# Performance work log

Hardware: AMD Instinct MI355X
Metric: run time of the kernel (lower is better)

Reference implementation:

```python
import jax, jax.numpy as jnp
import numpy as np

D_MODEL = 1024
NUM_HEADS = 16
D_LATENT = 256
HEAD_DIM = D_MODEL // NUM_HEADS
BATCH = 2048
SEQ = 32


def setup_inputs() -> dict:
    key = jax.random.key(0)
    ks = jax.random.split(key, 9)
    s = 1.0 / np.sqrt(D_MODEL)
    sl = 1.0 / np.sqrt(D_LATENT)
    return {
        "x": jax.random.normal(ks[0], (BATCH, SEQ, D_MODEL), dtype=jnp.float32),
        "memory": jax.random.normal(ks[1], (BATCH, SEQ, D_LATENT), dtype=jnp.float32),
        "W_q": jax.random.normal(ks[2], (D_MODEL, D_MODEL), dtype=jnp.float32) * s,
        "W_k": jax.random.normal(ks[3], (D_MODEL, D_MODEL), dtype=jnp.float32) * s,
        "W_v": jax.random.normal(ks[4], (D_MODEL, D_MODEL), dtype=jnp.float32) * s,
        "W_o": jax.random.normal(ks[5], (D_MODEL, D_MODEL), dtype=jnp.float32) * s,
        "W_down_kv": jax.random.normal(ks[6], (D_MODEL, D_LATENT), dtype=jnp.float32) * s,
        "W_up_k": jax.random.normal(ks[7], (D_LATENT, D_MODEL), dtype=jnp.float32) * sl,
        "W_up_v": jax.random.normal(ks[8], (D_LATENT, D_MODEL), dtype=jnp.float32) * sl,
    }


def reference(x, memory, W_q, W_k, W_v, W_o, W_down_kv, W_up_k, W_up_v):
    B, S, _ = x.shape
    q = x @ W_q                     # [B,S,D]
    k = x @ W_k
    v = x @ W_v
    latent_kv = (k + v) @ W_down_kv  # [B,S,L]
    latent_kv = jnp.nan_to_num((latent_kv + memory) * 0.5)
    k_rec = latent_kv @ W_up_k       # [B,S,D]
    v_rec = latent_kv @ W_up_v
    # split heads: [B,H,S,hd]
    qh = q.reshape(B, S, NUM_HEADS, HEAD_DIM).transpose(0, 2, 1, 3)
    kh = k_rec.reshape(B, S, NUM_HEADS, HEAD_DIM).transpose(0, 2, 1, 3)
    vh = v_rec.reshape(B, S, NUM_HEADS, HEAD_DIM).transpose(0, 2, 1, 3)
    # NOTE: faithful to source — scale is sqrt(d_model), not sqrt(head_dim)
    scores = jnp.einsum("bhqd,bhkd->bhqk", qh, kh) / jnp.sqrt(jnp.float32(D_MODEL))
    scores = jnp.nan_to_num(scores, nan=0.0, posinf=10.0, neginf=-10.0)
    attn = jax.nn.softmax(scores, axis=-1)
    ctx = jnp.einsum("bhqk,bhkd->bhqd", attn, vh)
    ctx = ctx.transpose(0, 2, 1, 3).reshape(B, S, D_MODEL)
    out = ctx @ W_o
    return out, latent_kv
```

## Files before the change

### kernel.cpp

```cpp
#include <hip/hip_runtime.h>
#include <hip/hip_bf16.h>

typedef unsigned short u16;
typedef __attribute__((ext_vector_type(8))) __bf16 bf16x8;
typedef __attribute__((ext_vector_type(8))) unsigned short u16x8;
typedef __attribute__((ext_vector_type(4))) float floatx4;
typedef __attribute__((ext_vector_type(16))) float floatx16;

#define AS1 __attribute__((address_space(1)))
#define AS3 __attribute__((address_space(3)))

__device__ __forceinline__ u16 f2bf(float f) {
  unsigned u = __float_as_uint(f);
  u += 0x7fffu + ((u >> 16) & 1u);
  return (u16)(u >> 16);
}

__device__ __forceinline__ void g2lds16(const u16* g, u16* l) {
  __builtin_amdgcn_global_load_lds((AS1 void*)g, (AS3 void*)l, 16, 0, 0);
}

__global__ __launch_bounds__(256) void k_cvt_bf16(const float* __restrict__ s,
                                                  u16* __restrict__ d, long n) {
  long i = ((long)blockIdx.x * blockDim.x + threadIdx.x) * 8;
  long stride = (long)gridDim.x * blockDim.x * 8;
  for (; i < n; i += stride) {
    float4 a = *(const float4*)(s + i);
    float4 b = *(const float4*)(s + i + 4);
    u16x8 o;
    o[0] = f2bf(a.x); o[1] = f2bf(a.y); o[2] = f2bf(a.z); o[3] = f2bf(a.w);
    o[4] = f2bf(b.x); o[5] = f2bf(b.y); o[6] = f2bf(b.z); o[7] = f2bf(b.w);
    *(u16x8*)(d + i) = o;
  }
}

__global__ __launch_bounds__(256) void k_addcvt(const float* __restrict__ s0,
                                                const float* __restrict__ s1,
                                                u16* __restrict__ d, long n) {
  long i = ((long)blockIdx.x * blockDim.x + threadIdx.x) * 8;
  long stride = (long)gridDim.x * blockDim.x * 8;
  for (; i < n; i += stride) {
    float4 a0 = *(const float4*)(s0 + i);
    float4 a1 = *(const float4*)(s0 + i + 4);
    float4 b0 = *(const float4*)(s1 + i);
    float4 b1 = *(const float4*)(s1 + i + 4);
    u16x8 o;
    o[0] = f2bf(a0.x + b0.x); o[1] = f2bf(a0.y + b0.y);
    o[2] = f2bf(a0.z + b0.z); o[3] = f2bf(a0.w + b0.w);
    o[4] = f2bf(a1.x + b1.x); o[5] = f2bf(a1.y + b1.y);
    o[6] = f2bf(a1.z + b1.z); o[7] = f2bf(a1.w + b1.w);
    *(u16x8*)(d + i) = o;
  }
}

__global__ __launch_bounds__(256) void k_tcvt(const float* __restrict__ s,
                                              u16* __restrict__ d, int R, int C) {
  __shared__ float t[32][33];
  const int lx = threadIdx.x, ly = threadIdx.y;
  const int bx = blockIdx.x * 32;
  const int by = blockIdx.y * 32;
  #pragma unroll
  for (int i = 0; i < 32; i += 8)
    t[ly + i][lx] = s[(size_t)(by + ly + i) * C + bx + lx];
  __syncthreads();
  #pragma unroll
  for (int i = 0; i < 32; i += 8)
    d[(size_t)(bx + ly + i) * R + by + lx] = f2bf(t[lx][ly + i]);
}


#define MFMA16(a, b, c) c = __builtin_amdgcn_mfma_f32_16x16x32_bf16(a, b, c, 0, 0, 0)

#define STAGE(BUF, OP, RH, T) do {                                              \
    const u16* Gp_ = (OP) ? Bg : Ag;                                            \
    const u16* g0_ = Gp_ + (size_t)((RH) * 128 + srow) * K + (T) * 64 + scols;  \
    u16* L_ = ldsb + ((BUF) * 2 + (OP)) * 16384 + (RH) * 8192 + tid * 8;        \
    g2lds16(g0_, L_);                                                           \
    g2lds16(g0_ + (size_t)64 * K, L_ + 4096);                                   \
  } while (0)

#define RD_A(AI, F, KS) \
  (*(const bf16x8*)(LA + ((wr * 128 + (AI) * 64 + (F) * 16 + fr) * 64 + ((((KS) * 32) + g8) ^ xr))))
#define RD_B(BJ, NF, KS) \
  (*(const bf16x8*)(LB + ((wc * 64 + (BJ) * 32 + (NF) * 16 + fr) * 64 + ((((KS) * 32) + g8) ^ xr))))

#define PHASE_READS(AI, BJ)                                                       \
  bf16x8 pa0_0 = RD_A(AI, 0, 0), pa1_0 = RD_A(AI, 1, 0);                          \
  bf16x8 pa2_0 = RD_A(AI, 2, 0), pa3_0 = RD_A(AI, 3, 0);                          \
  bf16x8 pa0_1 = RD_A(AI, 0, 1), pa1_1 = RD_A(AI, 1, 1);                          \
  bf16x8 pa2_1 = RD_A(AI, 2, 1), pa3_1 = RD_A(AI, 3, 1);                          \
  bf16x8 pb0_0 = RD_B(BJ, 0, 0), pb1_0 = RD_B(BJ, 1, 0);                          \
  bf16x8 pb0_1 = RD_B(BJ, 0, 1), pb1_1 = RD_B(BJ, 1, 1)

#define PHASE_MFMA(AI, BJ)                                                        \
  __builtin_amdgcn_s_setprio(1);                                                  \
  MFMA16(pa0_0, pb0_0, acc[(AI)*4 + 0][(BJ)*2 + 0]);                              \
  MFMA16(pa1_0, pb0_0, acc[(AI)*4 + 1][(BJ)*2 + 0]);                              \
  MFMA16(pa2_0, pb0_0, acc[(AI)*4 + 2][(BJ)*2 + 0]);                              \
  MFMA16(pa3_0, pb0_0, acc[(AI)*4 + 3][(BJ)*2 + 0]);                              \
  MFMA16(pa0_0, pb1_0, acc[(AI)*4 + 0][(BJ)*2 + 1]);                              \
  MFMA16(pa1_0, pb1_0, acc[(AI)*4 + 1][(BJ)*2 + 1]);                              \
  MFMA16(pa2_0, pb1_0, acc[(AI)*4 + 2][(BJ)*2 + 1]);                              \
  MFMA16(pa3_0, pb1_0, acc[(AI)*4 + 3][(BJ)*2 + 1]);                              \
  MFMA16(pa0_1, pb0_1, acc[(AI)*4 + 0][(BJ)*2 + 0]);                              \
  MFMA16(pa1_1, pb0_1, acc[(AI)*4 + 1][(BJ)*2 + 0]);                              \
  MFMA16(pa2_1, pb0_1, acc[(AI)*4 + 2][(BJ)*2 + 0]);                              \
  MFMA16(pa3_1, pb0_1, acc[(AI)*4 + 3][(BJ)*2 + 0]);                              \
  MFMA16(pa0_1, pb1_1, acc[(AI)*4 + 0][(BJ)*2 + 1]);                              \
  MFMA16(pa1_1, pb1_1, acc[(AI)*4 + 1][(BJ)*2 + 1]);                              \
  MFMA16(pa2_1, pb1_1, acc[(AI)*4 + 2][(BJ)*2 + 1]);                              \
  MFMA16(pa3_1, pb1_1, acc[(AI)*4 + 3][(BJ)*2 + 1]);                              \
  __builtin_amdgcn_s_setprio(0)

template <int MODE>
__global__ __launch_bounds__(512, 2) void gemm8p(
    const u16* __restrict__ A, const u16* __restrict__ Bt,
    int M, int N, int K, int ntn,
    u16* __restrict__ Cb, float* __restrict__ Cf,
    const float* __restrict__ memp, float* __restrict__ latf, u16* __restrict__ latb) {
  extern __shared__ u16 ldsb[];
  const int tid = threadIdx.x;
  const int lane = tid & 63;
  const int wid = tid >> 6;
  const int wr = wid >> 2, wc = wid & 3;

  int bid = blockIdx.x;
  {
    const int nwg = gridDim.x;
    const int q = nwg >> 3, r = nwg & 7;
    const int xcd = bid & 7, idx = bid >> 3;
    bid = (xcd < r ? xcd * (q + 1) : r * (q + 1) + (xcd - r) * q) + idx;
  }
  const int mt = bid / ntn, nt = bid % ntn;
  const int m0 = mt * 256, n0 = nt * 256;
  const int NT = K >> 6;

  const int srow = tid >> 3;
  const int scols = ((tid & 7) ^ (srow & 7)) * 8;
  const int fr = lane & 15;
  const int g8 = (lane >> 4) * 8;
  const int xr = (lane & 7) * 8;

  const u16* Ag = A + (size_t)m0 * K;
  const u16* Bg = Bt + (size_t)n0 * K;

  floatx4 acc[8][4];
  #pragma unroll
  for (int i = 0; i < 8; i++)
    #pragma unroll
    for (int j = 0; j < 4; j++) acc[i][j] = 0.0f;

  STAGE(0, 0, 0, 0);
  STAGE(0, 0, 1, 0);
  STAGE(0, 1, 0, 0);
  STAGE(0, 1, 1, 0);
  if (NT > 1) {
    STAGE(1, 0, 0, 1);
    asm volatile("s_waitcnt vmcnt(2)" ::: "memory");
  } else {
    asm volatile("s_waitcnt vmcnt(0)" ::: "memory");
  }
  __builtin_amdgcn_s_barrier();

  for (int t = 0; t < NT; ++t) {
    const int cur = t & 1;
    const u16* LA = ldsb + cur * 32768;
    const u16* LB = LA + 16384;
    const int nxt = cur ^ 1;
    {
      PHASE_READS(0, 0);
      if (t + 1 < NT) STAGE(nxt, 0, 1, t + 1);
      __builtin_amdgcn_s_barrier();
      asm volatile("s_waitcnt lgkmcnt(0)" ::: "memory");
      PHASE_MFMA(0, 0);
      __builtin_amdgcn_s_barrier();
    }
    {
      PHASE_READS(0, 1);
      if (t + 1 < NT) STAGE(nxt, 1, 0, t + 1);
      __builtin_amdgcn_s_barrier();
      asm volatile("s_waitcnt lgkmcnt(0)" ::: "memory");
      PHASE_MFMA(0, 1);
      __builtin_amdgcn_s_barrier();
    }
    {
      PHASE_READS(1, 0);
      if (t + 1 < NT) STAGE(nxt, 1, 1, t + 1);
      __builtin_amdgcn_s_barrier();
      asm volatile("s_waitcnt lgkmcnt(0)" ::: "memory");
      PHASE_MFMA(1, 0);
      __builtin_amdgcn_s_barrier();
    }
    {
      PHASE_READS(1, 1);
      asm volatile("s_waitcnt lgkmcnt(0)" ::: "memory");
      __builtin_amdgcn_s_barrier();
      if (t + 2 < NT) STAGE(cur, 0, 0, t + 2);
      PHASE_MFMA(1, 1);
      if (t + 2 < NT) asm volatile("s_waitcnt vmcnt(2)" ::: "memory");
      else            asm volatile("s_waitcnt vmcnt(0)" ::: "memory");
      __builtin_amdgcn_s_barrier();
    }
  }

  #pragma unroll
  for (int mi = 0; mi < 8; mi++) {
    const int mb = m0 + wr * 128 + mi * 16 + ((lane >> 4) * 4);
    #pragma unroll
    for (int ni = 0; ni < 4; ni++) {
      const int cb = n0 + wc * 64 + ni * 16 + (lane & 15);
      #pragma unroll
      for (int r = 0; r < 4; r++) {
        const int m = mb + r;
        const float v = acc[mi][ni][r];
        if (MODE == 0) {
          Cb[(size_t)m * N + cb] = f2bf(v);
        } else if (MODE == 1) {
          if (n0 < 1024) {
            Cb[(size_t)m * 1024 + cb] = f2bf(v);
          } else {
            int lc = cb - 1024;
            float lv = (v + memp[(size_t)m * 256 + lc]) * 0.5f;
            latf[(size_t)m * 256 + lc] = lv;
            latb[(size_t)m * 256 + lc] = f2bf(lv);
          }
        } else {
          Cf[(size_t)m * N + cb] = v;
        }
      }
    }
  }
}

__global__ __launch_bounds__(256) void k_attn(const u16* __restrict__ KV, u16* Q) {
  __shared__ u16 Qs[4][32][72];
  __shared__ u16 Ks[4][32][72];
  __shared__ u16 Vt[4][64][40];
  const int tid = threadIdx.x;
  const int hg = blockIdx.x;
  const int b = blockIdx.y;
  const long tok0 = (long)b * 32;

  {
    const int t = tid >> 3, ci = tid & 7;
    const int hd = ci >> 1, c0 = (ci & 1) * 32;
    const u16* qrow = Q + (tok0 + t) * 1024 + hg * 256 + ci * 32;
    #pragma unroll
    for (int u = 0; u < 4; u++)
      *(u16x8*)&Qs[hd][t][c0 + u * 8] = *(const u16x8*)(qrow + u * 8);
    const u16* krow = KV + (tok0 + t) * 2048 + hg * 256 + ci * 32;
    #pragma unroll
    for (int u = 0; u < 4; u++)
      *(u16x8*)&Ks[hd][t][c0 + u * 8] = *(const u16x8*)(krow + u * 8);
    const u16* vrow = KV + (tok0 + t) * 2048 + 1024 + hg * 256 + ci * 32;
    #pragma unroll
    for (int u = 0; u < 4; u++) {
      u16x8 v = *(const u16x8*)(vrow + u * 8);
      #pragma unroll
      for (int j = 0; j < 8; j++) Vt[hd][c0 + u * 8 + j][t] = v[j];
    }
  }
  __syncthreads();

  const int w = tid >> 6;
  const int lane = tid & 63;
  const int col = lane & 31, hi = lane >> 5;

  floatx16 S;
  #pragma unroll
  for (int r = 0; r < 16; r++) S[r] = 0.0f;
  #pragma unroll
  for (int kc = 0; kc < 4; kc++) {
    bf16x8 aq = *(const bf16x8*)&Qs[w][col][kc * 16 + hi * 8];
    bf16x8 bk = *(const bf16x8*)&Ks[w][col][kc * 16 + hi * 8];
    S = __builtin_amdgcn_mfma_f32_32x32x16_bf16(aq, bk, S, 0, 0, 0);
  }

  u16* Pw = &Qs[w][0][0];
  float pr[16];
  #pragma unroll
  for (int r = 0; r < 16; r++) {
    float sc = S[r] * 0.03125f;
    float mx = sc;
    #pragma unroll
    for (int off = 16; off >= 1; off >>= 1) mx = fmaxf(mx, __shfl_xor(mx, off, 64));
    float e = __expf(sc - mx);
    float sm = e;
    #pragma unroll
    for (int off = 16; off >= 1; off >>= 1) sm += __shfl_xor(sm, off, 64);
    pr[r] = e / sm;
  }
  #pragma unroll
  for (int r = 0; r < 16; r++) {
    int row = (r & 3) + 8 * (r >> 2) + 4 * hi;
    Pw[row * 40 + col] = f2bf(pr[r]);
  }
  __syncthreads();

  floatx16 c0v, c1v;
  #pragma unroll
  for (int r = 0; r < 16; r++) { c0v[r] = 0.0f; c1v[r] = 0.0f; }
  #pragma unroll
  for (int kc = 0; kc < 2; kc++) {
    bf16x8 ap = *(const bf16x8*)&Pw[col * 40 + kc * 16 + hi * 8];
    bf16x8 bv0 = *(const bf16x8*)&Vt[w][col][kc * 16 + hi * 8];
    bf16x8 bv1 = *(const bf16x8*)&Vt[w][32 + col][kc * 16 + hi * 8];
    c0v = __builtin_amdgcn_mfma_f32_32x32x16_bf16(ap, bv0, c0v, 0, 0, 0);
    c1v = __builtin_amdgcn_mfma_f32_32x32x16_bf16(ap, bv1, c1v, 0, 0, 0);
  }
  #pragma unroll
  for (int r = 0; r < 16; r++) {
    int row = (r & 3) + 8 * (r >> 2) + 4 * hi;
    u16* orow = Q + (tok0 + row) * 1024 + hg * 256 + w * 64;
    orow[col] = f2bf(c0v[r]);
    orow[col + 32] = f2bf(c1v[r]);
  }
}

extern "C" void kernel_launch(void* const* d_in, const int* in_sizes, int n_in,
                              void* d_out, int out_size, void* d_ws, size_t ws_size,
                              hipStream_t stream) {
  const float* x    = (const float*)d_in[0];
  const float* mem  = (const float*)d_in[1];
  const float* W_q  = (const float*)d_in[2];
  const float* W_k  = (const float*)d_in[3];
  const float* W_v  = (const float*)d_in[4];
  const float* W_o  = (const float*)d_in[5];
  const float* W_dn = (const float*)d_in[6];
  const float* W_uk = (const float*)d_in[7];
  const float* W_uv = (const float*)d_in[8];
  float* out  = (float*)d_out;
  float* latf = out + (size_t)67108864;

  char* wp = (char*)d_ws;
  u16* Qb  = (u16*)wp; wp += (size_t)65536 * 1024 * 2;
  u16* Lb  = (u16*)wp; wp += (size_t)65536 * 256 * 2;
  u16* WAt = (u16*)wp; wp += (size_t)1280 * 1024 * 2;
  u16* WBt = (u16*)wp; wp += (size_t)2048 * 256 * 2;
  u16* Wot = (u16*)wp; wp += (size_t)1024 * 1024 * 2;
  u16* Wdt = (u16*)wp; wp += (size_t)256 * 1024 * 2;
  u16* Wkv = (u16*)wp; wp += (size_t)1024 * 1024 * 2;

  u16* Xb  = (u16*)d_out;
  u16* KVb = (u16*)d_out;

  (void)hipFuncSetAttribute(reinterpret_cast<const void*>(&gemm8p<0>),
                            hipFuncAttributeMaxDynamicSharedMemorySize, 131072);
  (void)hipFuncSetAttribute(reinterpret_cast<const void*>(&gemm8p<1>),
                            hipFuncAttributeMaxDynamicSharedMemorySize, 131072);
  (void)hipFuncSetAttribute(reinterpret_cast<const void*>(&gemm8p<2>),
                            hipFuncAttributeMaxDynamicSharedMemorySize, 131072);

  dim3 b256(256);
  dim3 b512(512);
  dim3 tb(32, 8);
  k_cvt_bf16<<<4096, b256, 0, stream>>>(x, Xb, (long)67108864);
  k_addcvt<<<512, b256, 0, stream>>>(W_k, W_v, Wkv, (long)1048576);
  k_tcvt<<<dim3(32, 32), tb, 0, stream>>>(W_q, WAt, 1024, 1024);
  k_tcvt<<<dim3(8, 32),  tb, 0, stream>>>(W_dn, Wdt, 1024, 256);
  k_tcvt<<<dim3(32, 8),  tb, 0, stream>>>(W_uk, WBt, 256, 1024);
  k_tcvt<<<dim3(32, 8),  tb, 0, stream>>>(W_uv, WBt + (size_t)1024 * 256, 256, 1024);
  k_tcvt<<<dim3(32, 32), tb, 0, stream>>>(W_o, Wot, 1024, 1024);

  gemm8p<0><<<4, b512, 131072, stream>>>(
      Wdt, Wkv, 256, 1024, 1024, 4, WAt + (size_t)1024 * 1024,
      nullptr, nullptr, nullptr, nullptr);

  gemm8p<1><<<1280, b512, 131072, stream>>>(
      Xb, WAt, 65536, 1280, 1024, 5, Qb, nullptr, mem, latf, Lb);

  gemm8p<0><<<2048, b512, 131072, stream>>>(
      Lb, WBt, 65536, 2048, 256, 8, KVb, nullptr, nullptr, nullptr, nullptr);

  k_attn<<<dim3(4, 2048), b256, 0, stream>>>(KVb, Qb);

  gemm8p<2><<<1024, b512, 131072, stream>>>(
      Qb, Wot, 65536, 1024, 1024, 4, nullptr, out, nullptr, nullptr, nullptr);
}
```

Baseline: 887.4 us.

## Hold B fragments in registers across phases and issue all next-tile loads upfront

Restructures the GEMM main loop so each wave reads its full set of B fragments once per K-tile and keeps them in registers. Each of the four phases now only reads two new A row-fragments, which cuts redundant LDS reads of B. The global-to-LDS prefetch of all four quadrants of the next tile is issued at the start of the iteration instead of being spread across phases, and the deeper two-tile prefetch (t+2 into the current buffer) is dropped. In exchange this raises register pressure and lowers the prefetch depth, which may expose global load latency at the end of each tile.

```diff
diff --git a/kernel.cpp b/kernel.cpp
--- a/kernel.cpp
+++ b/kernel.cpp
@@ -79,37 +79,29 @@
     g2lds16(g0_ + (size_t)64 * K, L_ + 4096);                                   \
   } while (0)
 
-#define RD_A(AI, F, KS) \
-  (*(const bf16x8*)(LA + ((wr * 128 + (AI) * 64 + (F) * 16 + fr) * 64 + ((((KS) * 32) + g8) ^ xr))))
-#define RD_B(BJ, NF, KS) \
-  (*(const bf16x8*)(LB + ((wc * 64 + (BJ) * 32 + (NF) * 16 + fr) * 64 + ((((KS) * 32) + g8) ^ xr))))
-
-#define PHASE_READS(AI, BJ)                                                       \
-  bf16x8 pa0_0 = RD_A(AI, 0, 0), pa1_0 = RD_A(AI, 1, 0);                          \
-  bf16x8 pa2_0 = RD_A(AI, 2, 0), pa3_0 = RD_A(AI, 3, 0);                          \
-  bf16x8 pa0_1 = RD_A(AI, 0, 1), pa1_1 = RD_A(AI, 1, 1);                          \
-  bf16x8 pa2_1 = RD_A(AI, 2, 1), pa3_1 = RD_A(AI, 3, 1);                          \
-  bf16x8 pb0_0 = RD_B(BJ, 0, 0), pb1_0 = RD_B(BJ, 1, 0);                          \
-  bf16x8 pb0_1 = RD_B(BJ, 0, 1), pb1_1 = RD_B(BJ, 1, 1)
-
-#define PHASE_MFMA(AI, BJ)                                                        \
-  __builtin_amdgcn_s_setprio(1);                                                  \
-  MFMA16(pa0_0, pb0_0, acc[(AI)*4 + 0][(BJ)*2 + 0]);                              \
-  MFMA16(pa1_0, pb0_0, acc[(AI)*4 + 1][(BJ)*2 + 0]);                              \
-  MFMA16(pa2_0, pb0_0, acc[(AI)*4 + 2][(BJ)*2 + 0]);                              \
-  MFMA16(pa3_0, pb0_0, acc[(AI)*4 + 3][(BJ)*2 + 0]);                              \
-  MFMA16(pa0_0, pb1_0, acc[(AI)*4 + 0][(BJ)*2 + 1]);                              \
-  MFMA16(pa1_0, pb1_0, acc[(AI)*4 + 1][(BJ)*2 + 1]);                              \
-  MFMA16(pa2_0, pb1_0, acc[(AI)*4 + 2][(BJ)*2 + 1]);                              \
-  MFMA16(pa3_0, pb1_0, acc[(AI)*4 + 3][(BJ)*2 + 1]);                              \
-  MFMA16(pa0_1, pb0_1, acc[(AI)*4 + 0][(BJ)*2 + 0]);                              \
-  MFMA16(pa1_1, pb0_1, acc[(AI)*4 + 1][(BJ)*2 + 0]);                              \
-  MFMA16(pa2_1, pb0_1, acc[(AI)*4 + 2][(BJ)*2 + 0]);                              \
-  MFMA16(pa3_1, pb0_1, acc[(AI)*4 + 3][(BJ)*2 + 0]);                              \
-  MFMA16(pa0_1, pb1_1, acc[(AI)*4 + 0][(BJ)*2 + 1]);                              \
-  MFMA16(pa1_1, pb1_1, acc[(AI)*4 + 1][(BJ)*2 + 1]);                              \
-  MFMA16(pa2_1, pb1_1, acc[(AI)*4 + 2][(BJ)*2 + 1]);                              \
-  MFMA16(pa3_1, pb1_1, acc[(AI)*4 + 3][(BJ)*2 + 1]);                              \
+#define RD_A2(MI, KS) \
+  (*(const bf16x8*)(LA + ((wr * 128 + (MI) * 16 + fr) * 64 + ((((KS) * 32) + g8) ^ xr))))
+#define RD_B2(NI, KS) \
+  (*(const bf16x8*)(LB + ((wc * 64 + (NI) * 16 + fr) * 64 + ((((KS) * 32) + g8) ^ xr))))
+
+#define PH_MFMA(MI0)                                         \
+  __builtin_amdgcn_s_setprio(1);                             \
+  MFMA16(a0[0], Br[0][0], acc[MI0][0]);                      \
+  MFMA16(a1[0], Br[0][0], acc[(MI0) + 1][0]);                \
+  MFMA16(a0[0], Br[1][0], acc[MI0][1]);                      \
+  MFMA16(a1[0], Br[1][0], acc[(MI0) + 1][1]);                \
+  MFMA16(a0[0], Br[2][0], acc[MI0][2]);                      \
+  MFMA16(a1[0], Br[2][0], acc[(MI0) + 1][2]);                \
+  MFMA16(a0[0], Br[3][0], acc[MI0][3]);                      \
+  MFMA16(a1[0], Br[3][0], acc[(MI0) + 1][3]);                \
+  MFMA16(a0[1], Br[0][1], acc[MI0][0]);                      \
+  MFMA16(a1[1], Br[0][1], acc[(MI0) + 1][0]);                \
+  MFMA16(a0[1], Br[1][1], acc[MI0][1]);                      \
+  MFMA16(a1[1], Br[1][1], acc[(MI0) + 1][1]);                \
+  MFMA16(a0[1], Br[2][1], acc[MI0][2]);                      \
+  MFMA16(a1[1], Br[2][1], acc[(MI0) + 1][2]);                \
+  MFMA16(a0[1], Br[3][1], acc[MI0][3]);                      \
+  MFMA16(a1[1], Br[3][1], acc[(MI0) + 1][3]);                \
   __builtin_amdgcn_s_setprio(0)
 
 template <int MODE>
@@ -154,51 +146,56 @@
   STAGE(0, 0, 1, 0);
   STAGE(0, 1, 0, 0);
   STAGE(0, 1, 1, 0);
-  if (NT > 1) {
-    STAGE(1, 0, 0, 1);
-    asm volatile("s_waitcnt vmcnt(2)" ::: "memory");
-  } else {
-    asm volatile("s_waitcnt vmcnt(0)" ::: "memory");
-  }
+  asm volatile("s_waitcnt vmcnt(0)" ::: "memory");
   __builtin_amdgcn_s_barrier();
 
   for (int t = 0; t < NT; ++t) {
     const int cur = t & 1;
+    const int nxt = cur ^ 1;
     const u16* LA = ldsb + cur * 32768;
     const u16* LB = LA + 16384;
-    const int nxt = cur ^ 1;
+    bf16x8 Br[4][2];
+    bf16x8 a0[2], a1[2];
     {
-      PHASE_READS(0, 0);
-      if (t + 1 < NT) STAGE(nxt, 0, 1, t + 1);
+      #pragma unroll
+      for (int n = 0; n < 4; n++) { Br[n][0] = RD_B2(n, 0); Br[n][1] = RD_B2(n, 1); }
+      a0[0] = RD_A2(0, 0); a0[1] = RD_A2(0, 1);
+      a1[0] = RD_A2(1, 0); a1[1] = RD_A2(1, 1);
+      if (t + 1 < NT) {
+        STAGE(nxt, 0, 0, t + 1);
+        STAGE(nxt, 0, 1, t + 1);
+        STAGE(nxt, 1, 0, t + 1);
+        STAGE(nxt, 1, 1, t + 1);
+      }
+      asm volatile("s_waitcnt lgkmcnt(8)" ::: "memory");
       __builtin_amdgcn_s_barrier();
       asm volatile("s_waitcnt lgkmcnt(0)" ::: "memory");
-      PHASE_MFMA(0, 0);
+      PH_MFMA(0);
       __builtin_amdgcn_s_barrier();
     }
     {
-      PHASE_READS(0, 1);
-      if (t + 1 < NT) STAGE(nxt, 1, 0, t + 1);
+      a0[0] = RD_A2(2, 0); a0[1] = RD_A2(2, 1);
+      a1[0] = RD_A2(3, 0); a1[1] = RD_A2(3, 1);
       __builtin_amdgcn_s_barrier();
       asm volatile("s_waitcnt lgkmcnt(0)" ::: "memory");
-      PHASE_MFMA(0, 1);
+      PH_MFMA(2);
       __builtin_amdgcn_s_barrier();
     }
     {
-      PHASE_READS(1, 0);
-      if (t + 1 < NT) STAGE(nxt, 1, 1, t + 1);
+      a0[0] = RD_A2(4, 0); a0[1] = RD_A2(4, 1);
+      a1[0] = RD_A2(5, 0); a1[1] = RD_A2(5, 1);
       __builtin_amdgcn_s_barrier();
       asm volatile("s_waitcnt lgkmcnt(0)" ::: "memory");
-      PHASE_MFMA(1, 0);
+      PH_MFMA(4);
       __builtin_amdgcn_s_barrier();
     }
     {
-      PHASE_READS(1, 1);
+      a0[0] = RD_A2(6, 0); a0[1] = RD_A2(6, 1);
+      a1[0] = RD_A2(7, 0); a1[1] = RD_A2(7, 1);
+      __builtin_amdgcn_s_barrier();
       asm volatile("s_waitcnt lgkmcnt(0)" ::: "memory");
-      __builtin_amdgcn_s_barrier();
-      if (t + 2 < NT) STAGE(cur, 0, 0, t + 2);
-      PHASE_MFMA(1, 1);
-      if (t + 2 < NT) asm volatile("s_waitcnt vmcnt(2)" ::: "memory");
-      else            asm volatile("s_waitcnt vmcnt(0)" ::: "memory");
+      PH_MFMA(6);
+      asm volatile("s_waitcnt vmcnt(0)" ::: "memory");
       __builtin_amdgcn_s_barrier();
     }
   }
```

Result: no change. 893.5 us (+0.7%).
